# Performance work log

Hardware: AMD Instinct MI355X
Metric: run time of the kernel (lower is better)

The kernel has to match this reference:

```python
import jax, jax.numpy as jnp
import numpy as np

D = 1024       # d_model
DR = 1024      # d_rec
FFN = 4096     # ffn_inner
K = 4          # conv_kernel
B, T = 2, 4096
CHUNK = 64
EPS = 1e-6


def setup_inputs() -> dict:
    key = jax.random.key(0)
    ks = jax.random.split(key, 8)
    s = lambda k, shape, scale: jax.random.normal(k, shape, jnp.float32) * scale
    db = np.zeros((DR,), np.float32)
    q = DR // 4
    db[:q] = -2.2
    db[q:3 * q] = 0.0
    db[3 * q:] = 4.6
    return {
        "x": s(ks[0], (B, T, D), 1.0),
        "pre_norm_w": jnp.ones((D,), jnp.float32),
        "conv_w": s(ks[1], (D, 1, K), 0.3),
        "conv_b": jnp.zeros((D,), jnp.float32),
        "w_a": s(ks[2], (DR, D), 0.02),
        "w_i": s(ks[3], (DR, D), 0.02),
        "w_v": s(ks[4], (DR, D), 0.02),
        "out_proj_w": s(ks[5], (D, DR), 0.02),
        "decay_bias": jnp.asarray(db),
        "ffn_norm_w": jnp.ones((D,), jnp.float32),
        "w_gate_up": s(ks[6], (2 * FFN, D), 0.02),
        "w_down": s(ks[7], (D, FFN), 0.02),
    }


def rmsnorm(x, w):
    return x * jax.lax.rsqrt(jnp.mean(x * x, axis=-1, keepdims=True) + EPS) * w


def lin(x, w):  # nn.Linear weight layout (out, in)
    return jnp.einsum('btd,od->bto', x, w)


def causal_conv(h, w, b):
    # depthwise causal conv: h (B,T,D), w (D,1,K)
    hc = jnp.transpose(h, (0, 2, 1))  # (B,D,T)
    out = jax.lax.conv_general_dilated(
        hc, w, window_strides=(1,), padding=[(K - 1, 0)],
        dimension_numbers=('NCH', 'OIH', 'NCH'), feature_group_count=D)
    return jnp.transpose(out, (0, 2, 1)) + b


def chunked_scan(a, v):
    b, s, d = a.shape
    pad = (-s) % CHUNK
    af = jnp.pad(a, ((0, 0), (0, pad), (0, 0)), constant_values=1.0)
    vf = jnp.pad(v, ((0, 0), (0, pad), (0, 0)))
    n = (s + pad) // CHUNK
    dc = af.reshape(b, n, CHUNK, d)
    vc = vf.reshape(b, n, CHUNK, d)
    cum_decay = jnp.exp(jnp.cumsum(jnp.log(jnp.clip(dc, 1e-10)), axis=2))
    intra = cum_decay * jnp.cumsum(vc / jnp.clip(cum_decay, 1e-10), axis=2)

    def step(state, xs):
        cd, it = xs  # (B,CHUNK,d) each
        cs = it + cd * state[:, None, :]
        return cs[:, -1], cs

    _, states = jax.lax.scan(
        step, jnp.zeros((b, d), jnp.float32),
        (jnp.transpose(cum_decay, (1, 0, 2, 3)), jnp.transpose(intra, (1, 0, 2, 3))))
    return jnp.transpose(states, (1, 0, 2, 3)).reshape(b, n * CHUNK, d)[:, :s]


def reference(x, pre_norm_w, conv_w, conv_b, w_a, w_i, w_v, out_proj_w,
              decay_bias, ffn_norm_w, w_gate_up, w_down):
    h = rmsnorm(x, pre_norm_w)
    h = causal_conv(h, conv_w, conv_b)
    a = jax.nn.sigmoid(lin(h, w_a) + decay_bias)
    i_gate = jax.nn.sigmoid(lin(h, w_i))
    v = lin(h, w_v)
    input_signal = jnp.sqrt(jnp.clip(1.0 - a * a, 1e-8)) * (i_gate * v)
    rec_out = chunked_scan(a, input_signal).astype(x.dtype)
    x = x + lin(rec_out, out_proj_w)
    hn = rmsnorm(x, ffn_norm_w)
    gu = lin(hn, w_gate_up)
    gate, up = gu[..., :FFN], gu[..., FFN:]
    x = x + lin(jax.nn.silu(gate) * up, w_down)
    return x
```

## Files before the change

### kernel.cpp

```cpp
#include <hip/hip_runtime.h>

typedef __bf16 bf16_t;
typedef bf16_t bf16x4 __attribute__((ext_vector_type(4)));
typedef bf16_t bf16x8 __attribute__((ext_vector_type(8)));
typedef float f32x4 __attribute__((ext_vector_type(4)));

#define DD 1024
#define TT 4096

__device__ __forceinline__ void gload16(const void* g, void* l) {
    __builtin_amdgcn_global_load_lds(
        (const __attribute__((address_space(1))) void*)g,
        (__attribute__((address_space(3))) void*)l, 16, 0, 0);
}

__global__ __launch_bounds__(256) void cvt_bf16_k(const float* __restrict__ s,
                                                  bf16_t* __restrict__ d, int n) {
    int i = (blockIdx.x * 256 + threadIdx.x) * 4;
    if (i < n) {
        const float4 v = *(const float4*)(s + i);
        bf16x4 o;
        o[0] = (bf16_t)v.x; o[1] = (bf16_t)v.y; o[2] = (bf16_t)v.z; o[3] = (bf16_t)v.w;
        *(bf16x4*)(d + i) = o;
    }
}

__global__ __launch_bounds__(256) void cvt_ileave_k(const float* __restrict__ s0,
                                                    const float* __restrict__ s1,
                                                    bf16_t* __restrict__ d, int total) {
    int i = (blockIdx.x * 256 + threadIdx.x) * 4;
    if (i < total) {
        const int rp = i >> 10, k = i & 1023;
        const int c = rp >> 1;
        const float* src = ((rp & 1) ? s1 : s0) + (long)c * 1024 + k;
        const float4 v = *(const float4*)src;
        bf16x4 o;
        o[0] = (bf16_t)v.x; o[1] = (bf16_t)v.y; o[2] = (bf16_t)v.z; o[3] = (bf16_t)v.w;
        *(bf16x4*)(d + i) = o;
    }
}

__global__ __launch_bounds__(256) void rmsnorm_k(const float* __restrict__ x,
                                                 const float* __restrict__ w,
                                                 bf16_t* __restrict__ ob) {
    const long row = blockIdx.x;
    const float* xr = x + row * DD;
    const int t4 = threadIdx.x * 4;
    float4 v = *(const float4*)(xr + t4);
    float s = v.x*v.x + v.y*v.y + v.z*v.z + v.w*v.w;
    #pragma unroll
    for (int off = 1; off < 64; off <<= 1) s += __shfl_xor(s, off);
    __shared__ float red[4];
    if ((threadIdx.x & 63) == 0) red[threadIdx.x >> 6] = s;
    __syncthreads();
    float tot = red[0] + red[1] + red[2] + red[3];
    float sc = rsqrtf(tot * (1.0f / DD) + 1e-6f);
    float4 wv = *(const float4*)(w + t4);
    bf16x4 o;
    o[0] = (bf16_t)(v.x*sc*wv.x); o[1] = (bf16_t)(v.y*sc*wv.y);
    o[2] = (bf16_t)(v.z*sc*wv.z); o[3] = (bf16_t)(v.w*sc*wv.w);
    *(bf16x4*)(ob + row * DD + t4) = o;
}

__global__ __launch_bounds__(256) void conv_k(const bf16_t* __restrict__ h,
                                              const float* __restrict__ cw,
                                              const float* __restrict__ cb,
                                              bf16_t* __restrict__ hc) {
    const long idx = (long)blockIdx.x * 256 + threadIdx.x;
    const int d = (int)(idx & (DD - 1));
    const long bt = idx >> 10;
    const int t = (int)(bt & (TT - 1));
    const float w0 = cw[d*4+0], w1 = cw[d*4+1], w2 = cw[d*4+2], w3 = cw[d*4+3];
    const bf16_t* hp = h + bt * DD + d;
    float acc = cb[d] + (float)hp[0] * w3;
    if (t >= 1) acc += (float)hp[-DD]     * w2;
    if (t >= 2) acc += (float)hp[-2*DD]   * w1;
    if (t >= 3) acc += (float)hp[-3*DD]   * w0;
    hc[idx] = (bf16_t)acc;
}

__global__ __launch_bounds__(256) void scan1_k(const float* __restrict__ ap,
                                               const float* __restrict__ sp,
                                               float* __restrict__ cd63,
                                               float* __restrict__ i63) {
    const int d = blockIdx.x * 256 + threadIdx.x;
    const int c = blockIdx.y;
    const int b = blockIdx.z;
    const long rowbase = (long)b * TT + (long)c * 64;
    float la = 0.0f, rs = 0.0f, cdv = 0.0f, it = 0.0f;
    for (int t = 0; t < 64; t++) {
        const long off = (rowbase + t) * DD + d;
        const float a = ap[off];
        const float s = sp[off];
        const float sig = sqrtf(fmaxf(1.0f - a * a, 1e-8f)) * s;
        la += __logf(fmaxf(a, 1e-10f));
        cdv = __expf(la);
        rs += sig / fmaxf(cdv, 1e-10f);
        it = cdv * rs;
    }
    const long o = ((long)b * 64 + c) * DD + d;
    cd63[o] = cdv;
    i63[o]  = it;
}

__global__ __launch_bounds__(256) void scan2_k(const float* __restrict__ cd63,
                                               const float* __restrict__ i63,
                                               float* __restrict__ carry_in) {
    const int g = blockIdx.x * 256 + threadIdx.x;
    const int b = g >> 10, d = g & (DD - 1);
    float st = 0.0f;
    for (int c = 0; c < 64; c++) {
        const long o = ((long)b * 64 + c) * DD + d;
        carry_in[o] = st;
        st = i63[o] + cd63[o] * st;
    }
}

__global__ __launch_bounds__(256) void scan3_k(const float* __restrict__ ap,
                                               const float* __restrict__ sp,
                                               const float* __restrict__ carry_in,
                                               bf16_t* __restrict__ rec) {
    const int d = blockIdx.x * 256 + threadIdx.x;
    const int c = blockIdx.y;
    const int b = blockIdx.z;
    const long rowbase = (long)b * TT + (long)c * 64;
    const float carry = carry_in[((long)b * 64 + c) * DD + d];
    float la = 0.0f, rs = 0.0f;
    for (int t = 0; t < 64; t++) {
        const long off = (rowbase + t) * DD + d;
        const float a = ap[off];
        const float s = sp[off];
        const float sig = sqrtf(fmaxf(1.0f - a * a, 1e-8f)) * s;
        la += __logf(fmaxf(a, 1e-10f));
        const float cdv = __expf(la);
        rs += sig / fmaxf(cdv, 1e-10f);
        rec[off] = (bf16_t)(cdv * rs + cdv * carry);
    }
}

enum { EPI_SIGB = 0, EPI_ADDRES = 1, EPI_IV = 2, EPI_GU = 3 };

template<int EPI, int NREP>
__global__ __launch_bounds__(512, 2) void gemm4p_k(const bf16_t* __restrict__ Ag,
                                                   const bf16_t* __restrict__ Bg,
                                                   int M, int N, int K,
                                                   float* outF, bf16_t* outB,
                                                   const float* aux, int ldc) {
    constexpr int BN  = NREP * 64;
    constexpr int ASZ = 16384;
    constexpr int BSZ = BN * 64;
    constexpr int BUF = ASZ + BSZ;
    extern __shared__ bf16_t smem[];
    const int tid = threadIdx.x;
    const int l = tid & 63;
    const int w = tid >> 6;
    const int wm = w >> 2, wn = w & 3;

    const int gx = gridDim.x;
    const int gy = gridDim.y;
    const int lin = blockIdx.y * gx + blockIdx.x;
    long row0, col0;
    if ((gy & 7) == 0) {
        const int rpc = gy >> 3;
        const int q = lin >> 3;
        row0 = (long)((lin & 7) * rpc + q % rpc) * 256;
        col0 = (long)(q / rpc) * (long)BN;
    } else {
        row0 = (long)blockIdx.y * 256;
        col0 = (long)blockIdx.x * BN;
    }

    const int srow = l >> 3;
    const int scol = ((l & 7) ^ srow) * 8;
    const long aBase = row0 + srow;
    const long bBase = col0 + srow;
    const int R0a = w * 32;
    const int R0b = w * (BN / 8);

    const int NT = K >> 6;
    f32x4 acc[8][NREP] = {};

    const int lq2 = (l >> 4) * 16;
    const int rA = wm * 128 + (l & 15);
    const int rB = wn * (NREP * 16) + (l & 15);
    const int eA0 = rA * 64 + ((lq2 ^ ((rA & 7) << 4)) >> 1);
    const int eB0 = ASZ + rB * 64 + ((lq2 ^ ((rB & 7) << 4)) >> 1);

    #define ST_A(tt, off, i)                                                        \
        gload16(Ag + (aBase + R0a + (i) * 8) * (long)K + (long)(tt) * 64 + scol,    \
                &smem[(off) + (R0a + (i) * 8) * 64])
    #define ST_B(tt, off, i)                                                        \
        gload16(Bg + (bBase + R0b + (i) * 8) * (long)K + (long)(tt) * 64 + scol,    \
                &smem[(off) + ASZ + (R0b + (i) * 8) * 64])
    #define BAR asm volatile("s_barrier" ::: "memory")

    #pragma unroll
    for (int i = 0; i < NREP; i++) ST_B(0, 0, i);
    #pragma unroll
    for (int i = 0; i < 4; i++)    ST_A(0, 0, i);
    #pragma unroll
    for (int i = 0; i < NREP; i++) ST_B(1, BUF, i);
    if constexpr (NREP == 4) { asm volatile("s_waitcnt vmcnt(4)" ::: "memory"); }
    else                     { asm volatile("s_waitcnt vmcnt(2)" ::: "memory"); }
    BAR;

    for (int t = 0; t < NT; t++) {
        const int cur = (t & 1) * BUF;
        const int oth = BUF - cur;
        bf16x8 bk0[NREP], bk1[NREP], af[4];

        #pragma unroll
        for (int n = 0; n < NREP; n++)
            bk0[n] = *(const bf16x8*)&smem[cur + eB0 + n * 1024];
        #pragma unroll
        for (int m = 0; m < 4; m++)
            af[m] = *(const bf16x8*)&smem[cur + eA0 + m * 1024];
        if (t + 1 < NT) { ST_A(t + 1, oth, 0); ST_A(t + 1, oth, 1); }
        BAR;
        __builtin_amdgcn_s_setprio(1);
        #pragma unroll
        for (int m = 0; m < 4; m++)
            #pragma unroll
            for (int n = 0; n < NREP; n++)
                acc[m][n] = __builtin_amdgcn_mfma_f32_16x16x32_bf16(af[m], bk0[n], acc[m][n], 0, 0, 0);
        __builtin_amdgcn_s_setprio(0);
        BAR;

        #pragma unroll
        for (int n = 0; n < NREP; n++)
            bk1[n] = *(const bf16x8*)&smem[cur + (eB0 ^ 32) + n * 1024];
        #pragma unroll
        for (int m = 0; m < 4; m++)
            af[m] = *(const bf16x8*)&smem[cur + (eA0 ^ 32) + m * 1024];
        if (t + 1 < NT) { ST_A(t + 1, oth, 2); ST_A(t + 1, oth, 3); }
        BAR;
        __builtin_amdgcn_s_setprio(1);
        #pragma unroll
        for (int m = 0; m < 4; m++)
            #pragma unroll
            for (int n = 0; n < NREP; n++)
                acc[m][n] = __builtin_amdgcn_mfma_f32_16x16x32_bf16(af[m], bk1[n], acc[m][n], 0, 0, 0);
        __builtin_amdgcn_s_setprio(0);
        BAR;

        #pragma unroll
        for (int m = 0; m < 4; m++)
            af[m] = *(const bf16x8*)&smem[cur + eA0 + 4096 + m * 1024];
        if (t + 2 < NT) { ST_B(t + 2, cur, 0); ST_B(t + 2, cur, 1); }
        BAR;
        __builtin_amdgcn_s_setprio(1);
        #pragma unroll
        for (int m = 0; m < 4; m++)
            #pragma unroll
            for (int n = 0; n < NREP; n++)
                acc[m + 4][n] = __builtin_amdgcn_mfma_f32_16x16x32_bf16(af[m], bk0[n], acc[m + 4][n], 0, 0, 0);
        __builtin_amdgcn_s_setprio(0);
        BAR;

        #pragma unroll
        for (int m = 0; m < 4; m++)
            af[m] = *(const bf16x8*)&smem[cur + (eA0 ^ 32) + 4096 + m * 1024];
        if (t + 2 < NT) {
            if constexpr (NREP == 4) { ST_B(t + 2, cur, 2); ST_B(t + 2, cur, 3); }
            if constexpr (NREP == 4) { asm volatile("s_waitcnt vmcnt(4)" ::: "memory"); }
            else                     { asm volatile("s_waitcnt vmcnt(2)" ::: "memory"); }
        } else {
            asm volatile("s_waitcnt vmcnt(0)" ::: "memory");
        }
        BAR;
        __builtin_amdgcn_s_setprio(1);
        #pragma unroll
        for (int m = 0; m < 4; m++)
            #pragma unroll
            for (int n = 0; n < NREP; n++)
                acc[m + 4][n] = __builtin_amdgcn_mfma_f32_16x16x32_bf16(af[m], bk1[n], acc[m + 4][n], 0, 0, 0);
        __builtin_amdgcn_s_setprio(0);
        BAR;
    }
    #undef ST_A
    #undef ST_B
    #undef BAR

    #pragma unroll
    for (int m = 0; m < 8; m++) {
        const long r0 = row0 + wm * 128 + m * 16 + (l >> 4) * 4;
        #pragma unroll
        for (int n = 0; n < NREP; n++) {
            const long cc = col0 + wn * (NREP * 16) + n * 16 + (l & 15);
            f32x4 v = acc[m][n];
            #pragma unroll
            for (int j = 0; j < 4; j++) {
                const long r = r0 + j;
                const float xv = v[j];
                if (EPI == EPI_SIGB) {
                    outF[r * ldc + cc] = 1.0f / (1.0f + __expf(-(xv + aux[cc])));
                } else if (EPI == EPI_ADDRES) {
                    outF[r * ldc + cc] = xv + aux[r * ldc + cc];
                } else if (EPI == EPI_IV) {
                    const float px = __shfl_xor(xv, 1);
                    if ((l & 1) == 0)
                        outF[r * ldc + (cc >> 1)] = px / (1.0f + __expf(-xv));
                } else {
                    const float px = __shfl_xor(xv, 1);
                    if ((l & 1) == 0)
                        outB[r * ldc + (cc >> 1)] = (bf16_t)(xv / (1.0f + __expf(-xv)) * px);
                }
            }
        }
    }
}

extern "C" void kernel_launch(void* const* d_in, const int* in_sizes, int n_in,
                              void* d_out, int out_size, void* d_ws, size_t ws_size,
                              hipStream_t stream) {
    const float* x   = (const float*)d_in[0];
    const float* pnw = (const float*)d_in[1];
    const float* cw  = (const float*)d_in[2];
    const float* cb  = (const float*)d_in[3];
    const float* wa  = (const float*)d_in[4];
    const float* wi  = (const float*)d_in[5];
    const float* wv  = (const float*)d_in[6];
    const float* wop = (const float*)d_in[7];
    const float* db  = (const float*)d_in[8];
    const float* fnw = (const float*)d_in[9];
    const float* wgu = (const float*)d_in[10];
    const float* wdn = (const float*)d_in[11];
    float* out = (float*)d_out;

    char* ws = (char*)d_ws;
    bf16_t* wab   = (bf16_t*)(ws + 0);
    bf16_t* wivb  = (bf16_t*)(ws + 2097152);
    bf16_t* wopb  = (bf16_t*)(ws + 6291456);
    bf16_t* wgub  = (bf16_t*)(ws + 8388608);
    bf16_t* wdnb  = (bf16_t*)(ws + 25165824);
    bf16_t* hb    = (bf16_t*)(ws + 33554432);
    bf16_t* hn    = hb;
    bf16_t* hc    = (bf16_t*)(ws + 50331648);
    bf16_t* rec   = hc;
    float*  a_p   = (float*)(ws + 67108864);
    float*  s_p   = (float*)(ws + 100663296);
    bf16_t* act   = (bf16_t*)(ws + 67108864);
    float*  cd63  = (float*)(ws + 134217728);
    float*  i63   = (float*)(ws + 134742016);
    float*  carry = (float*)(ws + 135266304);

    const int LDS4 = 131072;
    const int LDS2 = 98304;
    hipFuncSetAttribute((const void*)gemm4p_k<EPI_SIGB, 2>,   hipFuncAttributeMaxDynamicSharedMemorySize, LDS2);
    hipFuncSetAttribute((const void*)gemm4p_k<EPI_IV, 4>,     hipFuncAttributeMaxDynamicSharedMemorySize, LDS4);
    hipFuncSetAttribute((const void*)gemm4p_k<EPI_ADDRES, 2>, hipFuncAttributeMaxDynamicSharedMemorySize, LDS2);
    hipFuncSetAttribute((const void*)gemm4p_k<EPI_GU, 4>,     hipFuncAttributeMaxDynamicSharedMemorySize, LDS4);

    cvt_bf16_k  <<<1024, 256, 0, stream>>>(wa,  wab,  1048576);
    cvt_ileave_k<<<2048, 256, 0, stream>>>(wi,  wv, wivb, 2097152);
    cvt_bf16_k  <<<1024, 256, 0, stream>>>(wop, wopb, 1048576);
    cvt_ileave_k<<<8192, 256, 0, stream>>>(wgu, wgu + 4194304, wgub, 8388608);
    cvt_bf16_k  <<<4096, 256, 0, stream>>>(wdn, wdnb, 4194304);

    rmsnorm_k<<<8192, 256, 0, stream>>>(x, pnw, hb);
    conv_k<<<32768, 256, 0, stream>>>(hb, cw, cb, hc);

    gemm4p_k<EPI_SIGB, 2><<<dim3(8, 32), 512, LDS2, stream>>>(hc, wab,  8192, 1024, 1024,
                                                              a_p, nullptr, db, 1024);
    gemm4p_k<EPI_IV, 4>  <<<dim3(8, 32), 512, LDS4, stream>>>(hc, wivb, 8192, 2048, 1024,
                                                              s_p, nullptr, nullptr, 1024);
    scan1_k<<<dim3(4, 64, 2), 256, 0, stream>>>(a_p, s_p, cd63, i63);
    scan2_k<<<8, 256, 0, stream>>>(cd63, i63, carry);
    scan3_k<<<dim3(4, 64, 2), 256, 0, stream>>>(a_p, s_p, carry, rec);

    gemm4p_k<EPI_ADDRES, 2><<<dim3(8, 32), 512, LDS2, stream>>>(rec, wopb, 8192, 1024, 1024,
                                                                out, nullptr, x, 1024);
    rmsnorm_k<<<8192, 256, 0, stream>>>(out, fnw, hn);
    gemm4p_k<EPI_GU, 4><<<dim3(32, 32), 512, LDS4, stream>>>(hn, wgub, 8192, 8192, 1024,
                                                             nullptr, act, nullptr, 4096);
    gemm4p_k<EPI_ADDRES, 2><<<dim3(8, 32), 512, LDS2, stream>>>(act, wdnb, 8192, 1024, 4096,
                                                                out, nullptr, out, 1024);
}
```

Before: 478.3 us.

## Switch GEMMs to 128x128 tiles with 256 threads and fuse a/iv projections

Replaces the 256xBN, 512-thread double-buffered GEMM with a 128x128-tile, 256-thread variant. It uses 64KB of LDS so two blocks can share a CU, and it simplifies the per-K-step schedule to two MFMA phases. The separate decay-gate and input/value projections are merged into one launch over a 3072-wide N dimension. This relies on the bf16 weight buffers sitting next to each other in the workspace, with the epilogue branching on the column index. The smaller tiles give more blocks per GEMM for better CU occupancy and fewer launches, but lower data reuse per tile and add more global-to-LDS traffic.

```diff
diff --git a/kernel.cpp b/kernel.cpp
--- a/kernel.cpp
+++ b/kernel.cpp
@@ -138,23 +138,22 @@
     }
 }
 
-enum { EPI_SIGB = 0, EPI_ADDRES = 1, EPI_IV = 2, EPI_GU = 3 };
-
-template<int EPI, int NREP>
-__global__ __launch_bounds__(512, 2) void gemm4p_k(const bf16_t* __restrict__ Ag,
+enum { EPI_AIV = 0, EPI_ADDRES = 1, EPI_GU = 2 };
+
+template<int EPI>
+__global__ __launch_bounds__(256, 2) void gemm2b_k(const bf16_t* __restrict__ Ag,
                                                    const bf16_t* __restrict__ Bg,
                                                    int M, int N, int K,
-                                                   float* outF, bf16_t* outB,
+                                                   float* outF, float* outF2,
+                                                   bf16_t* outB,
                                                    const float* aux, int ldc) {
-    constexpr int BN  = NREP * 64;
-    constexpr int ASZ = 16384;
-    constexpr int BSZ = BN * 64;
-    constexpr int BUF = ASZ + BSZ;
+    constexpr int ASZ = 8192;
+    constexpr int BUF = 16384;
     extern __shared__ bf16_t smem[];
     const int tid = threadIdx.x;
     const int l = tid & 63;
     const int w = tid >> 6;
-    const int wm = w >> 2, wn = w & 3;
+    const int wm = w >> 1, wn = w & 1;
 
     const int gx = gridDim.x;
     const int gy = gridDim.y;
@@ -163,143 +162,118 @@
     if ((gy & 7) == 0) {
         const int rpc = gy >> 3;
         const int q = lin >> 3;
-        row0 = (long)((lin & 7) * rpc + q % rpc) * 256;
-        col0 = (long)(q / rpc) * (long)BN;
+        row0 = (long)((lin & 7) * rpc + q % rpc) * 128;
+        col0 = (long)(q / rpc) * 128;
     } else {
-        row0 = (long)blockIdx.y * 256;
-        col0 = (long)blockIdx.x * BN;
+        row0 = (long)blockIdx.y * 128;
+        col0 = (long)blockIdx.x * 128;
     }
 
     const int srow = l >> 3;
     const int scol = ((l & 7) ^ srow) * 8;
     const long aBase = row0 + srow;
     const long bBase = col0 + srow;
-    const int R0a = w * 32;
-    const int R0b = w * (BN / 8);
+    const int R0 = w * 32;
 
     const int NT = K >> 6;
-    f32x4 acc[8][NREP] = {};
+    f32x4 acc[4][4] = {};
 
     const int lq2 = (l >> 4) * 16;
-    const int rA = wm * 128 + (l & 15);
-    const int rB = wn * (NREP * 16) + (l & 15);
+    const int rA = wm * 64 + (l & 15);
+    const int rB = wn * 64 + (l & 15);
     const int eA0 = rA * 64 + ((lq2 ^ ((rA & 7) << 4)) >> 1);
     const int eB0 = ASZ + rB * 64 + ((lq2 ^ ((rB & 7) << 4)) >> 1);
 
     #define ST_A(tt, off, i)                                                        \
-        gload16(Ag + (aBase + R0a + (i) * 8) * (long)K + (long)(tt) * 64 + scol,    \
-                &smem[(off) + (R0a + (i) * 8) * 64])
+        gload16(Ag + (aBase + R0 + (i) * 8) * (long)K + (long)(tt) * 64 + scol,     \
+                &smem[(off) + (R0 + (i) * 8) * 64])
     #define ST_B(tt, off, i)                                                        \
-        gload16(Bg + (bBase + R0b + (i) * 8) * (long)K + (long)(tt) * 64 + scol,    \
-                &smem[(off) + ASZ + (R0b + (i) * 8) * 64])
+        gload16(Bg + (bBase + R0 + (i) * 8) * (long)K + (long)(tt) * 64 + scol,     \
+                &smem[(off) + ASZ + (R0 + (i) * 8) * 64])
     #define BAR asm volatile("s_barrier" ::: "memory")
 
     #pragma unroll
-    for (int i = 0; i < NREP; i++) ST_B(0, 0, i);
-    #pragma unroll
-    for (int i = 0; i < 4; i++)    ST_A(0, 0, i);
-    #pragma unroll
-    for (int i = 0; i < NREP; i++) ST_B(1, BUF, i);
-    if constexpr (NREP == 4) { asm volatile("s_waitcnt vmcnt(4)" ::: "memory"); }
-    else                     { asm volatile("s_waitcnt vmcnt(2)" ::: "memory"); }
+    for (int i = 0; i < 4; i++) ST_B(0, 0, i);
+    #pragma unroll
+    for (int i = 0; i < 4; i++) ST_A(0, 0, i);
+    #pragma unroll
+    for (int i = 0; i < 4; i++) ST_B(1, BUF, i);
+    asm volatile("s_waitcnt vmcnt(4)" ::: "memory");
     BAR;
 
     for (int t = 0; t < NT; t++) {
         const int cur = (t & 1) * BUF;
         const int oth = BUF - cur;
-        bf16x8 bk0[NREP], bk1[NREP], af[4];
-
-        #pragma unroll
-        for (int n = 0; n < NREP; n++)
-            bk0[n] = *(const bf16x8*)&smem[cur + eB0 + n * 1024];
+        bf16x8 bk[4], af[4];
+
+        #pragma unroll
+        for (int n = 0; n < 4; n++)
+            bk[n] = *(const bf16x8*)&smem[cur + eB0 + n * 1024];
         #pragma unroll
         for (int m = 0; m < 4; m++)
             af[m] = *(const bf16x8*)&smem[cur + eA0 + m * 1024];
-        if (t + 1 < NT) { ST_A(t + 1, oth, 0); ST_A(t + 1, oth, 1); }
+        if (t + 1 < NT) {
+            #pragma unroll
+            for (int i = 0; i < 4; i++) ST_A(t + 1, oth, i);
+        }
         BAR;
         __builtin_amdgcn_s_setprio(1);
         #pragma unroll
         for (int m = 0; m < 4; m++)
             #pragma unroll
-            for (int n = 0; n < NREP; n++)
-                acc[m][n] = __builtin_amdgcn_mfma_f32_16x16x32_bf16(af[m], bk0[n], acc[m][n], 0, 0, 0);
+            for (int n = 0; n < 4; n++)
+                acc[m][n] = __builtin_amdgcn_mfma_f32_16x16x32_bf16(af[m], bk[n], acc[m][n], 0, 0, 0);
         __builtin_amdgcn_s_setprio(0);
         BAR;
 
         #pragma unroll
-        for (int n = 0; n < NREP; n++)
-            bk1[n] = *(const bf16x8*)&smem[cur + (eB0 ^ 32) + n * 1024];
+        for (int n = 0; n < 4; n++)
+            bk[n] = *(const bf16x8*)&smem[cur + (eB0 ^ 32) + n * 1024];
         #pragma unroll
         for (int m = 0; m < 4; m++)
             af[m] = *(const bf16x8*)&smem[cur + (eA0 ^ 32) + m * 1024];
-        if (t + 1 < NT) { ST_A(t + 1, oth, 2); ST_A(t + 1, oth, 3); }
         BAR;
         __builtin_amdgcn_s_setprio(1);
         #pragma unroll
         for (int m = 0; m < 4; m++)
             #pragma unroll
-            for (int n = 0; n < NREP; n++)
-                acc[m][n] = __builtin_amdgcn_mfma_f32_16x16x32_bf16(af[m], bk1[n], acc[m][n], 0, 0, 0);
+            for (int n = 0; n < 4; n++)
+                acc[m][n] = __builtin_amdgcn_mfma_f32_16x16x32_bf16(af[m], bk[n], acc[m][n], 0, 0, 0);
         __builtin_amdgcn_s_setprio(0);
-        BAR;
-
-        #pragma unroll
-        for (int m = 0; m < 4; m++)
-            af[m] = *(const bf16x8*)&smem[cur + eA0 + 4096 + m * 1024];
-        if (t + 2 < NT) { ST_B(t + 2, cur, 0); ST_B(t + 2, cur, 1); }
-        BAR;
-        __builtin_amdgcn_s_setprio(1);
-        #pragma unroll
-        for (int m = 0; m < 4; m++)
-            #pragma unroll
-            for (int n = 0; n < NREP; n++)
-                acc[m + 4][n] = __builtin_amdgcn_mfma_f32_16x16x32_bf16(af[m], bk0[n], acc[m + 4][n], 0, 0, 0);
-        __builtin_amdgcn_s_setprio(0);
-        BAR;
-
-        #pragma unroll
-        for (int m = 0; m < 4; m++)
-            af[m] = *(const bf16x8*)&smem[cur + (eA0 ^ 32) + 4096 + m * 1024];
         if (t + 2 < NT) {
-            if constexpr (NREP == 4) { ST_B(t + 2, cur, 2); ST_B(t + 2, cur, 3); }
-            if constexpr (NREP == 4) { asm volatile("s_waitcnt vmcnt(4)" ::: "memory"); }
-            else                     { asm volatile("s_waitcnt vmcnt(2)" ::: "memory"); }
+            #pragma unroll
+            for (int i = 0; i < 4; i++) ST_B(t + 2, cur, i);
+            asm volatile("s_waitcnt vmcnt(4)" ::: "memory");
         } else {
             asm volatile("s_waitcnt vmcnt(0)" ::: "memory");
         }
         BAR;
-        __builtin_amdgcn_s_setprio(1);
-        #pragma unroll
-        for (int m = 0; m < 4; m++)
-            #pragma unroll
-            for (int n = 0; n < NREP; n++)
-                acc[m + 4][n] = __builtin_amdgcn_mfma_f32_16x16x32_bf16(af[m], bk1[n], acc[m + 4][n], 0, 0, 0);
-        __builtin_amdgcn_s_setprio(0);
-        BAR;
     }
     #undef ST_A
     #undef ST_B
     #undef BAR
 
     #pragma unroll
-    for (int m = 0; m < 8; m++) {
-        const long r0 = row0 + wm * 128 + m * 16 + (l >> 4) * 4;
-        #pragma unroll
-        for (int n = 0; n < NREP; n++) {
-            const long cc = col0 + wn * (NREP * 16) + n * 16 + (l & 15);
+    for (int m = 0; m < 4; m++) {
+        const long r0 = row0 + wm * 64 + m * 16 + (l >> 4) * 4;
+        #pragma unroll
+        for (int n = 0; n < 4; n++) {
+            const long cc = col0 + wn * 64 + n * 16 + (l & 15);
             f32x4 v = acc[m][n];
             #pragma unroll
             for (int j = 0; j < 4; j++) {
                 const long r = r0 + j;
                 const float xv = v[j];
-                if (EPI == EPI_SIGB) {
-                    outF[r * ldc + cc] = 1.0f / (1.0f + __expf(-(xv + aux[cc])));
+                if (EPI == EPI_AIV) {
+                    if (cc < 1024) {
+                        outF[r * ldc + cc] = 1.0f / (1.0f + __expf(-(xv + aux[cc])));
+                    } else {
+                        const float px = __shfl_xor(xv, 1);
+                        if ((l & 1) == 0)
+                            outF2[r * ldc + ((cc - 1024) >> 1)] = px / (1.0f + __expf(-xv));
+                    }
                 } else if (EPI == EPI_ADDRES) {
                     outF[r * ldc + cc] = xv + aux[r * ldc + cc];
-                } else if (EPI == EPI_IV) {
-                    const float px = __shfl_xor(xv, 1);
-                    if ((l & 1) == 0)
-                        outF[r * ldc + (cc >> 1)] = px / (1.0f + __expf(-xv));
                 } else {
                     const float px = __shfl_xor(xv, 1);
                     if ((l & 1) == 0)
@@ -344,12 +318,10 @@
     float*  i63   = (float*)(ws + 134742016);
     float*  carry = (float*)(ws + 135266304);
 
-    const int LDS4 = 131072;
-    const int LDS2 = 98304;
-    hipFuncSetAttribute((const void*)gemm4p_k<EPI_SIGB, 2>,   hipFuncAttributeMaxDynamicSharedMemorySize, LDS2);
-    hipFuncSetAttribute((const void*)gemm4p_k<EPI_IV, 4>,     hipFuncAttributeMaxDynamicSharedMemorySize, LDS4);
-    hipFuncSetAttribute((const void*)gemm4p_k<EPI_ADDRES, 2>, hipFuncAttributeMaxDynamicSharedMemorySize, LDS2);
-    hipFuncSetAttribute((const void*)gemm4p_k<EPI_GU, 4>,     hipFuncAttributeMaxDynamicSharedMemorySize, LDS4);
+    const int LDSB = 65536;
+    hipFuncSetAttribute((const void*)gemm2b_k<EPI_AIV>,    hipFuncAttributeMaxDynamicSharedMemorySize, LDSB);
+    hipFuncSetAttribute((const void*)gemm2b_k<EPI_ADDRES>, hipFuncAttributeMaxDynamicSharedMemorySize, LDSB);
+    hipFuncSetAttribute((const void*)gemm2b_k<EPI_GU>,     hipFuncAttributeMaxDynamicSharedMemorySize, LDSB);
 
     cvt_bf16_k  <<<1024, 256, 0, stream>>>(wa,  wab,  1048576);
     cvt_ileave_k<<<2048, 256, 0, stream>>>(wi,  wv, wivb, 2097152);
@@ -360,19 +332,17 @@
     rmsnorm_k<<<8192, 256, 0, stream>>>(x, pnw, hb);
     conv_k<<<32768, 256, 0, stream>>>(hb, cw, cb, hc);
 
-    gemm4p_k<EPI_SIGB, 2><<<dim3(8, 32), 512, LDS2, stream>>>(hc, wab,  8192, 1024, 1024,
-                                                              a_p, nullptr, db, 1024);
-    gemm4p_k<EPI_IV, 4>  <<<dim3(8, 32), 512, LDS4, stream>>>(hc, wivb, 8192, 2048, 1024,
-                                                              s_p, nullptr, nullptr, 1024);
+    gemm2b_k<EPI_AIV><<<dim3(24, 64), 256, LDSB, stream>>>(hc, wab, 8192, 3072, 1024,
+                                                           a_p, s_p, nullptr, db, 1024);
     scan1_k<<<dim3(4, 64, 2), 256, 0, stream>>>(a_p, s_p, cd63, i63);
     scan2_k<<<8, 256, 0, stream>>>(cd63, i63, carry);
     scan3_k<<<dim3(4, 64, 2), 256, 0, stream>>>(a_p, s_p, carry, rec);
 
-    gemm4p_k<EPI_ADDRES, 2><<<dim3(8, 32), 512, LDS2, stream>>>(rec, wopb, 8192, 1024, 1024,
-                                                                out, nullptr, x, 1024);
+    gemm2b_k<EPI_ADDRES><<<dim3(8, 64), 256, LDSB, stream>>>(rec, wopb, 8192, 1024, 1024,
+                                                             out, nullptr, nullptr, x, 1024);
     rmsnorm_k<<<8192, 256, 0, stream>>>(out, fnw, hn);
-    gemm4p_k<EPI_GU, 4><<<dim3(32, 32), 512, LDS4, stream>>>(hn, wgub, 8192, 8192, 1024,
-                                                             nullptr, act, nullptr, 4096);
-    gemm4p_k<EPI_ADDRES, 2><<<dim3(8, 32), 512, LDS2, stream>>>(act, wdnb, 8192, 1024, 4096,
-                                                                out, nullptr, out, 1024);
-}
+    gemm2b_k<EPI_GU><<<dim3(64, 64), 256, LDSB, stream>>>(hn, wgub, 8192, 8192, 1024,
+                                                          nullptr, nullptr, act, nullptr, 4096);
+    gemm2b_k<EPI_ADDRES><<<dim3(8, 64), 256, LDSB, stream>>>(act, wdnb, 8192, 1024, 4096,
+                                                             out, nullptr, nullptr, out, 1024);
+}
```

After: 484.0 us. No clear change (+1.2%).
